# Performance work log

Measured on AMD Instinct MI355X. Metric: run time of the kernel, lower is better.

## Reference

```python
import jax, jax.numpy as jnp
import numpy as np

DEPTH_CHANNEL = 48  # max_disp(192) / downsample_scale(4)


def setup_inputs() -> dict:
    key = jax.random.key(0)
    k1, k2 = jax.random.split(key)
    B, C, H, W = 4, 512, 96, 312
    left_features = jax.random.normal(k1, (B, C, H, W), dtype=jnp.float32)
    right_features = jax.random.normal(k2, (B, C, H, W), dtype=jnp.float32)
    return {"left_features": left_features, "right_features": right_features}


def reference(left_features, right_features):
    # PSM cosine cost volume: for each disparity i,
    #   cost[:, i, :, i:] = mean_c(left[:, :, :, i:] * right[:, :, :, :W-i])
    # positions w < i remain zero (from the pre-zeroed tensor in the original).
    B, C, H, W = left_features.shape
    planes = []
    for i in range(DEPTH_CHANNEL):  # small fixed disparity loop (48), unrolled under jit
        corr = jnp.mean(
            left_features[:, :, :, i:] * right_features[:, :, :, : W - i],
            axis=1,
        )  # [B, H, W-i]
        planes.append(jnp.pad(corr, ((0, 0), (0, 0), (i, 0))))  # zero-fill w < i
    return jnp.stack(planes, axis=1)  # [B, D, H, W]
```

## Files before the change

### kernel.cpp

```cpp
#include <hip/hip_runtime.h>
#include <hip/hip_bf16.h>
#include <stdint.h>


#define B_ 4
#define C_ 512
#define H_ 96
#define W_ 312
#define D_ 48
#define HW_ (H_ * W_)
#define CHW_ (C_ * HW_)

#define KC 64
#define NCHUNK (C_ / KC)
#define HALFW 156
#define LCOLS 160
#define RCOLS 208
#define PITCH 128
#define LBYTES (LCOLS * PITCH)
#define RBYTES (RCOLS * PITCH)
#define SMEM_BYTES (LBYTES + RBYTES)

typedef __bf16 bf16x8 __attribute__((ext_vector_type(8)));
typedef float  f32x4  __attribute__((ext_vector_type(4)));

__device__ __forceinline__ uint32_t pack2_bf16(float a, float b) {
    uint32_t ua = __builtin_bit_cast(uint32_t, a);
    uint32_t ub = __builtin_bit_cast(uint32_t, b);
    ua += 0x7FFFu + ((ua >> 16) & 1u);
    ub += 0x7FFFu + ((ub >> 16) & 1u);
    return (ua >> 16) | (ub & 0xFFFF0000u);
}

__global__ __launch_bounds__(512, 4)
void psm_cost_volume(const float* __restrict__ lf,
                     const float* __restrict__ rf,
                     float* __restrict__ out) {
    const int half = blockIdx.x;
    const int h    = blockIdx.y;
    const int b    = blockIdx.z;
    const int wb   = half * HALFW;
    const int tid  = threadIdx.x;
    const int lane = tid & 63;
    const int wave = tid >> 6;
    const int l15  = lane & 15;
    const int l4   = lane >> 4;

    extern __shared__ char smem[];

    const float* lbase = lf + (size_t)b * CHW_ + (size_t)h * W_;
    const float* rbase = rf + (size_t)b * CHW_ + (size_t)h * W_;

    f32x4 acc[5];
    #pragma unroll
    for (int i = 0; i < 5; ++i) acc[i] = f32x4{0.f, 0.f, 0.f, 0.f};

    for (int ch = 0; ch < NCHUNK; ++ch) {
        const int c0 = ch * KC;
        if (ch) __syncthreads();

        #pragma unroll
        for (int it = 0; it < 3; ++it) {
            int idx = tid + it * 512;
            if (idx < 32 * 40) {
                int rp = idx / 40;
                int q  = idx - rp * 40;
                int w4 = wb + 4 * q;
                f32x4 v0 = {0.f, 0.f, 0.f, 0.f}, v1 = {0.f, 0.f, 0.f, 0.f};
                if (w4 + 3 < W_) {
                    const float* g = lbase + (size_t)(c0 + 2 * rp) * HW_ + w4;
                    v0 = *(const f32x4*)g;
                    v1 = *(const f32x4*)(g + HW_);
                }
                const int cc    = 2 * rp;
                const int cbyte = (cc & 7) << 1;
                const int chi   = cc >> 3;
                #pragma unroll
                for (int j = 0; j < 4; ++j) {
                    int lw  = 4 * q + j;
                    int off = lw * PITCH + ((chi ^ (lw & 7)) << 4) + cbyte;
                    *(uint32_t*)(smem + off) = pack2_bf16(v0[j], v1[j]);
                }
            }
        }
        #pragma unroll
        for (int it = 0; it < 4; ++it) {
            int idx = tid + it * 512;
            if (idx < 32 * 52) {
                int rp = idx / 52;
                int q  = idx - rp * 52;
                int w4 = wb - 48 + 4 * q;
                f32x4 v0 = {0.f, 0.f, 0.f, 0.f}, v1 = {0.f, 0.f, 0.f, 0.f};
                if (w4 >= 0 && w4 + 3 < W_) {
                    const float* g = rbase + (size_t)(c0 + 2 * rp) * HW_ + w4;
                    v0 = *(const f32x4*)g;
                    v1 = *(const f32x4*)(g + HW_);
                }
                const int cc    = 2 * rp;
                const int cbyte = (cc & 7) << 1;
                const int chi   = cc >> 3;
                #pragma unroll
                for (int j = 0; j < 4; ++j) {
                    int lw  = 4 * q + j;
                    int off = LBYTES + lw * PITCH + ((chi ^ (lw & 7)) << 4) + cbyte;
                    *(uint32_t*)(smem + off) = pack2_bf16(v0[j], v1[j]);
                }
            }
        }
        __syncthreads();

        #pragma unroll
        for (int ks = 0; ks < 2; ++ks) {
            const int slot = ((ks * 4 + l4) ^ (l15 & 7)) << 4;
            #pragma unroll
            for (int pi = 0; pi < 5; ++pi) {
                const int p   = wave * 5 + pi;
                const int n   = p >> 2;
                const int jj  = p & 3;
                const int lwB = 16 * n + l15;
                const int lwA = 16 * (n + jj) + l15;
                bf16x8 afrag = *(const bf16x8*)(smem + LBYTES + lwA * PITCH + slot);
                bf16x8 bfrag = *(const bf16x8*)(smem + lwB * PITCH + slot);
                acc[pi] = __builtin_amdgcn_mfma_f32_16x16x32_bf16(afrag, bfrag, acc[pi], 0, 0, 0);
            }
        }
    }
    __syncthreads();

    float* outs = (float*)smem;
    #pragma unroll
    for (int pi = 0; pi < 5; ++pi) {
        const int p  = wave * 5 + pi;
        const int n  = p >> 2;
        const int jj = p & 3;
        const int lw = 16 * n + l15;
        #pragma unroll
        for (int r = 0; r < 4; ++r) {
            int tm = 4 * l4 + r;
            int d  = 48 - 16 * jj + l15 - tm;
            if (d >= 0 && d < D_ && lw < HALFW) {
                outs[d * HALFW + lw] = acc[pi][r] * (1.f / 512.f);
            }
        }
    }
    __syncthreads();

    float* obase = out + (size_t)b * (D_ * HW_) + (size_t)h * W_ + wb;
    for (int idx = tid; idx < D_ * HALFW; idx += 512) {
        int d  = idx / HALFW;
        int lw = idx - d * HALFW;
        obase[(size_t)d * HW_ + lw] = outs[idx];
    }
}

extern "C" void kernel_launch(void* const* d_in, const int* in_sizes, int n_in,
                              void* d_out, int out_size, void* d_ws, size_t ws_size,
                              hipStream_t stream) {
    const float* lf = (const float*)d_in[0];
    const float* rf = (const float*)d_in[1];
    float* out = (float*)d_out;
    dim3 grid(2, H_, B_);
    psm_cost_volume<<<grid, 512, SMEM_BYTES, stream>>>(lf, rf, out);
}
```

Baseline: 125.4 us.

## Use scalar coalesced loads with rotated LDS layout and per-wave fixed diagonal tiles

The global-to-LDS staging switches from float4 loads per thread (4 columns, strided stores) to scalar per-column loads, with consecutive threads covering consecutive columns. The LDS layout adds a dword rotation keyed on the 16-column group so that the stores avoid bank conflicts. Work is reassigned so each wave keeps one fixed diagonal offset jj and the A-fragment reads are templated per jj to undo the rotation. The aim is fewer LDS bank conflicts in staging and no divergent index math, at the cost of more, narrower global loads and split A-fragment reads for odd offsets.

```diff
diff --git a/kernel.cpp b/kernel.cpp
--- a/kernel.cpp
+++ b/kernel.cpp
@@ -23,6 +23,8 @@
 
 typedef __bf16 bf16x8 __attribute__((ext_vector_type(8)));
 typedef float  f32x4  __attribute__((ext_vector_type(4)));
+typedef uint32_t u32x2 __attribute__((ext_vector_type(2)));
+typedef uint32_t u32x4 __attribute__((ext_vector_type(4)));
 
 __device__ __forceinline__ uint32_t pack2_bf16(float a, float b) {
     uint32_t ua = __builtin_bit_cast(uint32_t, a);
@@ -30,6 +32,44 @@
     ua += 0x7FFFu + ((ua >> 16) & 1u);
     ub += 0x7FFFu + ((ub >> 16) & 1u);
     return (ua >> 16) | (ub & 0xFFFF0000u);
+}
+
+__device__ __forceinline__ int lds_off(int lw, int rp) {
+    return lw * PITCH + (((rp >> 2) ^ (lw & 7)) << 4)
+         + (((rp & 3) + ((lw >> 4) & 3)) & 3) * 4;
+}
+
+template<int JJ>
+__device__ __forceinline__ void compute_chunk(const char* smem, int l15, int l4,
+                                              int nb, f32x4* acc) {
+    #pragma unroll
+    for (int ks = 0; ks < 2; ++ks) {
+        const int chi  = ks * 4 + l4;
+        const int slot = (chi ^ (l15 & 7)) << 4;
+        #pragma unroll
+        for (int pi = 0; pi < 5; ++pi) {
+            const int n   = 2 * pi + nb;
+            const int lwB = 16 * n + l15;
+            const int lwA = lwB + 16 * JJ;
+            bf16x8 bfrag = *(const bf16x8*)(smem + lwB * PITCH + slot);
+            const char* ap = smem + LBYTES + lwA * PITCH + slot;
+            u32x4 av;
+            if constexpr (JJ == 0) {
+                av = *(const u32x4*)ap;
+            } else if constexpr (JJ == 2) {
+                u32x2 lo = *(const u32x2*)(ap + 8);
+                u32x2 hi = *(const u32x2*)(ap + 0);
+                av = u32x4{lo.x, lo.y, hi.x, hi.y};
+            } else {
+                av.x = *(const uint32_t*)(ap + (((0 + JJ) & 3) << 2));
+                av.y = *(const uint32_t*)(ap + (((1 + JJ) & 3) << 2));
+                av.z = *(const uint32_t*)(ap + (((2 + JJ) & 3) << 2));
+                av.w = *(const uint32_t*)(ap + (((3 + JJ) & 3) << 2));
+            }
+            bf16x8 afrag = __builtin_bit_cast(bf16x8, av);
+            acc[pi] = __builtin_amdgcn_mfma_f32_16x16x32_bf16(afrag, bfrag, acc[pi], 0, 0, 0);
+        }
+    }
 }
 
 __global__ __launch_bounds__(512, 4)
@@ -45,6 +85,8 @@
     const int wave = tid >> 6;
     const int l15  = lane & 15;
     const int l4   = lane >> 4;
+    const int jj   = wave & 3;
+    const int nb   = wave >> 2;
 
     extern __shared__ char smem[];
 
@@ -60,69 +102,40 @@
         if (ch) __syncthreads();
 
         #pragma unroll
-        for (int it = 0; it < 3; ++it) {
-            int idx = tid + it * 512;
-            if (idx < 32 * 40) {
-                int rp = idx / 40;
-                int q  = idx - rp * 40;
-                int w4 = wb + 4 * q;
-                f32x4 v0 = {0.f, 0.f, 0.f, 0.f}, v1 = {0.f, 0.f, 0.f, 0.f};
-                if (w4 + 3 < W_) {
-                    const float* g = lbase + (size_t)(c0 + 2 * rp) * HW_ + w4;
-                    v0 = *(const f32x4*)g;
-                    v1 = *(const f32x4*)(g + HW_);
-                }
-                const int cc    = 2 * rp;
-                const int cbyte = (cc & 7) << 1;
-                const int chi   = cc >> 3;
-                #pragma unroll
-                for (int j = 0; j < 4; ++j) {
-                    int lw  = 4 * q + j;
-                    int off = lw * PITCH + ((chi ^ (lw & 7)) << 4) + cbyte;
-                    *(uint32_t*)(smem + off) = pack2_bf16(v0[j], v1[j]);
-                }
+        for (int it = 0; it < 10; ++it) {
+            int idx = it * 512 + tid;
+            int rp  = idx / LCOLS;
+            int lw  = idx - rp * LCOLS;
+            int w4  = wb + lw;
+            float a0 = 0.f, a1 = 0.f;
+            if (w4 < W_) {
+                const float* g = lbase + (size_t)(c0 + 2 * rp) * HW_ + w4;
+                a0 = g[0];
+                a1 = g[HW_];
             }
+            *(uint32_t*)(smem + lds_off(lw, rp)) = pack2_bf16(a0, a1);
         }
         #pragma unroll
-        for (int it = 0; it < 4; ++it) {
-            int idx = tid + it * 512;
-            if (idx < 32 * 52) {
-                int rp = idx / 52;
-                int q  = idx - rp * 52;
-                int w4 = wb - 48 + 4 * q;
-                f32x4 v0 = {0.f, 0.f, 0.f, 0.f}, v1 = {0.f, 0.f, 0.f, 0.f};
-                if (w4 >= 0 && w4 + 3 < W_) {
-                    const float* g = rbase + (size_t)(c0 + 2 * rp) * HW_ + w4;
-                    v0 = *(const f32x4*)g;
-                    v1 = *(const f32x4*)(g + HW_);
-                }
-                const int cc    = 2 * rp;
-                const int cbyte = (cc & 7) << 1;
-                const int chi   = cc >> 3;
-                #pragma unroll
-                for (int j = 0; j < 4; ++j) {
-                    int lw  = 4 * q + j;
-                    int off = LBYTES + lw * PITCH + ((chi ^ (lw & 7)) << 4) + cbyte;
-                    *(uint32_t*)(smem + off) = pack2_bf16(v0[j], v1[j]);
-                }
+        for (int it = 0; it < 13; ++it) {
+            int idx = it * 512 + tid;
+            int rp  = idx / RCOLS;
+            int lw  = idx - rp * RCOLS;
+            int w4  = wb - 48 + lw;
+            float a0 = 0.f, a1 = 0.f;
+            if (w4 >= 0 && w4 < W_) {
+                const float* g = rbase + (size_t)(c0 + 2 * rp) * HW_ + w4;
+                a0 = g[0];
+                a1 = g[HW_];
             }
+            *(uint32_t*)(smem + LBYTES + lds_off(lw, rp)) = pack2_bf16(a0, a1);
         }
         __syncthreads();
 
-        #pragma unroll
-        for (int ks = 0; ks < 2; ++ks) {
-            const int slot = ((ks * 4 + l4) ^ (l15 & 7)) << 4;
-            #pragma unroll
-            for (int pi = 0; pi < 5; ++pi) {
-                const int p   = wave * 5 + pi;
-                const int n   = p >> 2;
-                const int jj  = p & 3;
-                const int lwB = 16 * n + l15;
-                const int lwA = 16 * (n + jj) + l15;
-                bf16x8 afrag = *(const bf16x8*)(smem + LBYTES + lwA * PITCH + slot);
-                bf16x8 bfrag = *(const bf16x8*)(smem + lwB * PITCH + slot);
-                acc[pi] = __builtin_amdgcn_mfma_f32_16x16x32_bf16(afrag, bfrag, acc[pi], 0, 0, 0);
-            }
+        switch (jj) {
+            case 0:  compute_chunk<0>(smem, l15, l4, nb, acc); break;
+            case 1:  compute_chunk<1>(smem, l15, l4, nb, acc); break;
+            case 2:  compute_chunk<2>(smem, l15, l4, nb, acc); break;
+            default: compute_chunk<3>(smem, l15, l4, nb, acc); break;
         }
     }
     __syncthreads();
@@ -130,9 +143,7 @@
     float* outs = (float*)smem;
     #pragma unroll
     for (int pi = 0; pi < 5; ++pi) {
-        const int p  = wave * 5 + pi;
-        const int n  = p >> 2;
-        const int jj = p & 3;
+        const int n  = 2 * pi + nb;
         const int lw = 16 * n + l15;
         #pragma unroll
         for (int r = 0; r < 4; ++r) {
```

New measurement: 226.5 us. 1.81x slower.
